# Performance work log

Measured on AMD Instinct MI355X. Metric: run time of the kernel, lower is better.

Reference implementation:

```python
import jax, jax.numpy as jnp
import numpy as np

B, N, C, E = 8, 4096, 128, 131072  # batch, nodes, channels (in==out), edges


def _linear_params(key, fan_in, fan_out):
    kw, kb = jax.random.split(key)
    s = 1.0 / np.sqrt(fan_in).astype(np.float32)
    W = jax.random.uniform(kw, (fan_in, fan_out), jnp.float32, -s, s)
    b = jax.random.uniform(kb, (fan_out,), jnp.float32, -s, s)
    return W, b


def setup_inputs() -> dict:
    key = jax.random.key(0)
    ks = jax.random.split(key, 6)
    x = jax.random.normal(ks[0], (B, N, C), jnp.float32)
    edge_index = jax.random.randint(ks[1], (2, E), 0, N, jnp.int64)
    W0, b0 = _linear_params(ks[2], C, C)        # lin0: in -> out
    W1, b1 = _linear_params(ks[3], 2 * C, C)    # lin1: 2*out -> out
    W2, b2 = _linear_params(ks[4], C, C)        # lin2: out -> out
    Wo, bo = _linear_params(ks[5], C, C)        # output: out -> out
    return {"x": x, "edge_index": edge_index, "W0": W0, "b0": b0,
            "W1": W1, "b1": b1, "W2": W2, "b2": b2, "Wo": Wo, "bo": bo}


def reference(x, edge_index, W0, b0, W1, b1, W2, b2, Wo, bo):
    n = x.shape[1]
    # symmetric 0/1 adjacency (duplicate edges collapse via .set), zero diagonal
    adj = jnp.zeros((n, n), x.dtype)
    adj = adj.at[edge_index[0], edge_index[1]].set(1.0)
    adj = adj.at[edge_index[1], edge_index[0]].set(1.0)
    diag = jnp.arange(n)
    adj = adj.at[diag, diag].set(0.0)
    h = x @ W0 + b0                               # [B, N, C]
    agg = jnp.einsum('ij,bjd->bid', adj, h)       # neighbor aggregation
    cat = jnp.concatenate([x, agg], axis=-1)      # [B, N, 2C]
    out = (cat @ W1 + b1) @ W2 + b2
    out = jax.nn.gelu(out, approximate=False) @ Wo + bo  # torch exact GELU
    return x + out
```

## Files before the change

kernel.cpp:

```cpp
#include <hip/hip_runtime.h>
#include <hip/hip_bf16.h>
#include <math.h>

#define NN 4096
#define BB 8
#define CC 128
#define EE 131072
#define M_ROWS (BB*NN)
#define DEG_CAP 512

typedef __attribute__((ext_vector_type(8))) short short8;
typedef __attribute__((ext_vector_type(4))) float f32x4;

__device__ __forceinline__ float bf2f(unsigned int u){
    union { unsigned int i; float f; } v; v.i = u << 16; return v.f;
}
__device__ __forceinline__ unsigned short f2bf(float f){
    union { float f; unsigned int i; } v; v.f = f;
    unsigned int u = v.i;
    unsigned int r = u + 0x7FFFu + ((u >> 16) & 1u);
    return (unsigned short)(r >> 16);
}

__device__ __forceinline__ int swz(int r, int k2 ){
    return r * 256 + (k2 ^ ((r & 7) << 4));
}

__global__ __launch_bounds__(256) void k_init(uint4* __restrict__ bits4,
                                              const float* __restrict__ x,
                                              unsigned short* __restrict__ xb,
                                              const float* __restrict__ W0, const float* __restrict__ W1,
                                              const float* __restrict__ W2, const float* __restrict__ Wo,
                                              unsigned short* __restrict__ Wt1a, unsigned short* __restrict__ Wt1b,
                                              unsigned short* __restrict__ Wt2,  unsigned short* __restrict__ Wto,
                                              unsigned short* __restrict__ W0bf){
    int bid = blockIdx.x, t = threadIdx.x;
    if (bid < 512){
        bits4[bid * 256 + t] = (uint4){0u, 0u, 0u, 0u};
        return;
    }
    if (bid < 2560){
        size_t e = (size_t)(bid - 512) * 2048 + t * 8;
        float4 lo = *((const float4*)(x + e));
        float4 hi = *((const float4*)(x + e + 4));
        ushort4 w0, w1;
        w0.x = f2bf(lo.x); w0.y = f2bf(lo.y); w0.z = f2bf(lo.z); w0.w = f2bf(lo.w);
        w1.x = f2bf(hi.x); w1.y = f2bf(hi.y); w1.z = f2bf(hi.z); w1.w = f2bf(hi.w);
        *((ushort4*)(xb + e)) = w0;
        *((ushort4*)(xb + e + 4)) = w1;
        return;
    }
    int idx = (bid - 2560) * 256 + t;
    int s = idx >> 14;
    int e = idx & 16383;
    int n = e >> 7, k = e & 127;
    float v; unsigned short* dst;
    switch (s){
        case 0:  v = W1[k*128+n];        dst = Wt1a; break;
        case 1:  v = W1[(128+k)*128+n];  dst = Wt1b; break;
        case 2:  v = W2[k*128+n];        dst = Wt2;  break;
        case 3:  v = Wo[k*128+n];        dst = Wto;  break;
        default: v = W0[n*128+k];        dst = W0bf; break;
    }
    dst[n*128+k] = f2bf(v);
}

__device__ __forceinline__ void stage_w(const unsigned short* __restrict__ Wt,
                                        unsigned short* Ws, int t){
    #pragma unroll
    for (int it = 0; it < 8; ++it){
        int g = it * 2048 + t * 8;
        int r = g >> 7, k = g & 127;
        uint4 v = *((const uint4*)(Wt + r * 128 + k));
        *((uint4*)((char*)Ws + swz(r, k * 2))) = v;
    }
}
__device__ __forceinline__ void stage_a_bf16(const unsigned short* __restrict__ src, int blockRow,
                                             unsigned short* As, int t){
    #pragma unroll
    for (int it = 0; it < 4; ++it){
        int g = it * 2048 + t * 8;
        int r = g >> 7, k = g & 127;
        uint4 v = *((const uint4*)(src + (size_t)(blockRow + r) * 128 + k));
        *((uint4*)((char*)As + swz(r, k * 2))) = v;
    }
}
__device__ __forceinline__ void mfma_pass(const unsigned short* As, const unsigned short* Ws,
                                          int wr, int wc, int l15, int lh, f32x4 acc[2][4]){
    #pragma unroll
    for (int ks = 0; ks < 4; ++ks){
        const int kc = ks * 32 + lh * 8;
        short8 af[2], bfv[4];
        #pragma unroll
        for (int m = 0; m < 2; m++){
            int r = wr + m * 16 + l15;
            af[m] = *((const short8*)((const char*)As + swz(r, kc * 2)));
        }
        #pragma unroll
        for (int n = 0; n < 4; n++){
            int r = wc + n * 16 + l15;
            bfv[n] = *((const short8*)((const char*)Ws + swz(r, kc * 2)));
        }
        #pragma unroll
        for (int m = 0; m < 2; m++)
            #pragma unroll
            for (int n = 0; n < 4; n++)
                acc[m][n] = __builtin_amdgcn_mfma_f32_16x16x32_bf16(af[m], bfv[n], acc[m][n], 0, 0, 0);
    }
}

__global__ __launch_bounds__(256) void k_scatter(const int* __restrict__ ei,
                                                 unsigned int* __restrict__ bits,
                                                 const unsigned short* __restrict__ W0bf,
                                                 const unsigned short* __restrict__ Wt1b,
                                                 const float* __restrict__ b0,
                                                 const float* __restrict__ W1,
                                                 unsigned short* __restrict__ Wtu,
                                                 float* __restrict__ c1){
    const int bid = blockIdx.x, t = threadIdx.x;
    if (bid < 512){
        int e = bid * 256 + t;
        int u = ei[e], v = ei[EE + e];
        atomicOr(&bits[u * 128 + (v >> 5)], 1u << (v & 31));
        atomicOr(&bits[v * 128 + (u >> 5)], 1u << (u & 31));
        return;
    }
    __shared__ unsigned short As[128*128];
    __shared__ unsigned short Ws[128*128];
    stage_w(W0bf, As, t);
    stage_w(Wt1b, Ws, t);
    __syncthreads();
    const int lane = t & 63, w = t >> 6;
    const int wr = w * 32;
    const int l15 = lane & 15, lh = lane >> 4;
    f32x4 acc[2][8];
    #pragma unroll
    for (int m = 0; m < 2; m++) for (int n = 0; n < 8; n++) acc[m][n] = (f32x4)(0.0f);
    #pragma unroll
    for (int ks = 0; ks < 4; ++ks){
        const int kc = ks * 32 + lh * 8;
        short8 af[2], bfv[8];
        #pragma unroll
        for (int m = 0; m < 2; m++){
            int r = wr + m * 16 + l15;
            af[m] = *((const short8*)((const char*)As + swz(r, kc * 2)));
        }
        #pragma unroll
        for (int n = 0; n < 8; n++){
            int r = n * 16 + l15;
            bfv[n] = *((const short8*)((const char*)Ws + swz(r, kc * 2)));
        }
        #pragma unroll
        for (int m = 0; m < 2; m++)
            #pragma unroll
            for (int n = 0; n < 8; n++)
                acc[m][n] = __builtin_amdgcn_mfma_f32_16x16x32_bf16(af[m], bfv[n], acc[m][n], 0, 0, 0);
    }
    #pragma unroll
    for (int m = 0; m < 2; m++){
        #pragma unroll
        for (int rr = 0; rr < 4; rr++){
            int r = wr + m * 16 + lh * 4 + rr;
            #pragma unroll
            for (int n = 0; n < 8; n++){
                int c = n * 16 + l15;
                Wtu[c * 128 + r] = f2bf(acc[m][n][rr]);
            }
        }
    }
    if (t < 128){
        float s = 0.f;
        #pragma unroll 8
        for (int k = 0; k < 128; k++)
            s += b0[k] * W1[(size_t)(128 + k) * 128 + t];
        c1[t] = s;
    }
}

__global__ __launch_bounds__(128) void k_csr(const unsigned int* __restrict__ bits,
                                             unsigned short* __restrict__ cols, int* __restrict__ deg){
    __shared__ int sc[128];
    int i = blockIdx.x, t = threadIdx.x;
    unsigned int w = bits[i * 128 + t];
    if (t == (i >> 5)) w &= ~(1u << (i & 31));
    int c = __popc(w);
    sc[t] = c; __syncthreads();
    int val = c;
    for (int off = 1; off < 128; off <<= 1){
        int add = (t >= off) ? sc[t - off] : 0;
        __syncthreads();
        val += add; sc[t] = val;
        __syncthreads();
    }
    int total = sc[127];
    int pos = val - c;
    unsigned int ww = w;
    while (ww){
        int b = __ffs(ww) - 1;
        ww &= ww - 1;
        if (pos < DEG_CAP) cols[(size_t)i * DEG_CAP + pos] = (unsigned short)(t * 32 + b);
        pos++;
    }
    if (t == 0) deg[i] = total < DEG_CAP ? total : DEG_CAP;
}

__device__ __forceinline__ void acc8u(uint4 u, float* a){
    a[0] += bf2f(u.x & 0xFFFFu); a[1] += bf2f(u.x >> 16);
    a[2] += bf2f(u.y & 0xFFFFu); a[3] += bf2f(u.y >> 16);
    a[4] += bf2f(u.z & 0xFFFFu); a[5] += bf2f(u.z >> 16);
    a[6] += bf2f(u.w & 0xFFFFu); a[7] += bf2f(u.w >> 16);
}

__global__ __launch_bounds__(256) void k_agg(const unsigned short* __restrict__ h,
                                             const unsigned short* __restrict__ cols,
                                             const int* __restrict__ deg,
                                             unsigned short* __restrict__ agg){
    __shared__ unsigned short scol[4][DEG_CAP];
    const int t = threadIdx.x;
    const int w = t >> 6, lane = t & 63;
    const int sub = lane >> 4, li = lane & 15;
    const int b = blockIdx.x & 7;
    const int i = ((blockIdx.x >> 3) << 2) + w;
    const int d = deg[i];
    const unsigned short* cl = cols + (size_t)i * DEG_CAP;
    for (int q = lane; q < d; q += 64) scol[w][q] = cl[q];

    const unsigned short* hb = h + (size_t)b * (NN*128) + li * 8;
    float a[8];
    #pragma unroll
    for (int c = 0; c < 8; c++) a[c] = 0.f;

    int n = sub;
    for (; n + 4 < d; n += 8){
        int j0 = scol[w][n], j1 = scol[w][n+4];
        uint4 u0 = *((const uint4*)(hb + ((size_t)j0 << 7)));
        uint4 u1 = *((const uint4*)(hb + ((size_t)j1 << 7)));
        acc8u(u0, a); acc8u(u1, a);
    }
    if (n < d){
        uint4 u0 = *((const uint4*)(hb + ((size_t)scol[w][n] << 7)));
        acc8u(u0, a);
    }
    #pragma unroll
    for (int c = 0; c < 8; c++){
        a[c] += __shfl_xor(a[c], 16);
        a[c] += __shfl_xor(a[c], 32);
    }
    if (sub == 0){
        uint4 o;
        o.x = (unsigned)f2bf(a[0]) | ((unsigned)f2bf(a[1]) << 16);
        o.y = (unsigned)f2bf(a[2]) | ((unsigned)f2bf(a[3]) << 16);
        o.z = (unsigned)f2bf(a[4]) | ((unsigned)f2bf(a[5]) << 16);
        o.w = (unsigned)f2bf(a[6]) | ((unsigned)f2bf(a[7]) << 16);
        *((uint4*)(agg + (size_t)b * (NN*128) + ((size_t)i << 7) + li * 8)) = o;
    }
}

__global__ __launch_bounds__(256) void k_mlp(const unsigned short* __restrict__ xb,
                                             const unsigned short* __restrict__ u,
                                             const unsigned short* __restrict__ Wt1a,
                                             const unsigned short* __restrict__ Wtu,
                                             const unsigned short* __restrict__ Wt2,
                                             const unsigned short* __restrict__ Wto,
                                             const float* __restrict__ c1,
                                             const float* __restrict__ b1,
                                             const float* __restrict__ b2,
                                             const float* __restrict__ bo,
                                             const int* __restrict__ deg,
                                             float* __restrict__ out){
    __shared__ unsigned short As[64*128];
    __shared__ unsigned short Ws[128*128];
    const int t = threadIdx.x;
    const int blockRow = blockIdx.x * 64;
    const int lane = t & 63, w = t >> 6;
    const int wr = (w >> 1) * 32, wc = (w & 1) * 64;
    const int l15 = lane & 15, lh = lane >> 4;

    f32x4 acc[2][4];
    #pragma unroll
    for (int m = 0; m < 2; m++) for (int n = 0; n < 4; n++) acc[m][n] = (f32x4)(0.0f);

    stage_a_bf16(xb, blockRow, As, t);
    stage_w(Wt1a, Ws, t);
    __syncthreads();
    mfma_pass(As, Ws, wr, wc, l15, lh, acc);

    f32x4 acc3[2][4];
    #pragma unroll
    for (int m = 0; m < 2; m++){
        #pragma unroll
        for (int rr = 0; rr < 4; rr++){
            int rl = wr + m * 16 + lh * 4 + rr;
            #pragma unroll
            for (int n = 0; n < 4; n++){
                int col = wc + n * 16 + l15;
                unsigned int us = *((const unsigned short*)((const char*)As + swz(rl, col * 2)));
                acc3[m][n][rr] = bf2f(us) + bo[col];
            }
        }
    }
    __syncthreads();

    stage_a_bf16(u, blockRow, As, t);
    stage_w(Wtu, Ws, t);
    __syncthreads();
    mfma_pass(As, Ws, wr, wc, l15, lh, acc);
    __syncthreads();

    #pragma unroll
    for (int m = 0; m < 2; m++){
        #pragma unroll
        for (int rr = 0; rr < 4; rr++){
            int rl = wr + m * 16 + lh * 4 + rr;
            int node = (blockRow + rl) & (NN - 1);
            float degf = (float)deg[node];
            #pragma unroll
            for (int n = 0; n < 4; n++){
                int col = wc + n * 16 + l15;
                float v = acc[m][n][rr] + b1[col] + degf * c1[col];
                *((unsigned short*)((char*)As + swz(rl, col * 2))) = f2bf(v);
            }
        }
    }
    stage_w(Wt2, Ws, t);
    __syncthreads();

    f32x4 acc2[2][4];
    #pragma unroll
    for (int m = 0; m < 2; m++) for (int n = 0; n < 4; n++) acc2[m][n] = (f32x4)(0.0f);
    mfma_pass(As, Ws, wr, wc, l15, lh, acc2);
    __syncthreads();

    #pragma unroll
    for (int m = 0; m < 2; m++){
        #pragma unroll
        for (int rr = 0; rr < 4; rr++){
            int rl = wr + m * 16 + lh * 4 + rr;
            #pragma unroll
            for (int n = 0; n < 4; n++){
                int col = wc + n * 16 + l15;
                float v = acc2[m][n][rr] + b2[col];
                v = 0.5f * v * (1.0f + erff(v * 0.70710678118f));
                *((unsigned short*)((char*)As + swz(rl, col * 2))) = f2bf(v);
            }
        }
    }
    stage_w(Wto, Ws, t);
    __syncthreads();

    mfma_pass(As, Ws, wr, wc, l15, lh, acc3);

    #pragma unroll
    for (int m = 0; m < 2; m++){
        #pragma unroll
        for (int rr = 0; rr < 4; rr++){
            int row = blockRow + wr + m * 16 + lh * 4 + rr;
            #pragma unroll
            for (int n = 0; n < 4; n++){
                int col = wc + n * 16 + l15;
                out[(size_t)row * 128 + col] = acc3[m][n][rr];
            }
        }
    }
}

extern "C" void kernel_launch(void* const* d_in, const int* in_sizes, int n_in,
                              void* d_out, int out_size, void* d_ws, size_t ws_size,
                              hipStream_t stream) {
    const float* x  = (const float*)d_in[0];
    const int*   ei = (const int*)d_in[1];
    const float* W0 = (const float*)d_in[2];
    const float* b0 = (const float*)d_in[3];
    const float* W1 = (const float*)d_in[4];
    const float* b1 = (const float*)d_in[5];
    const float* W2 = (const float*)d_in[6];
    const float* b2 = (const float*)d_in[7];
    const float* Wo = (const float*)d_in[8];
    const float* bo = (const float*)d_in[9];
    float* out = (float*)d_out;

    char* ws = (char*)d_ws;
    unsigned int* bits    = (unsigned int*)(ws + 0);
    unsigned short* cols  = (unsigned short*)(ws + 2097152);
    int*   deg            = (int*)(ws + 6291456);
    unsigned short* xb    = (unsigned short*)(ws + 6307840);
    unsigned short* ubuf  = (unsigned short*)(ws + 14696448);
    unsigned short* Wt1a  = (unsigned short*)(ws + 23085056);
    unsigned short* Wt1b  = (unsigned short*)(ws + 23085056 + 32768);
    unsigned short* Wt2   = (unsigned short*)(ws + 23085056 + 65536);
    unsigned short* Wto   = (unsigned short*)(ws + 23085056 + 98304);
    unsigned short* W0bf  = (unsigned short*)(ws + 23085056 + 131072);
    unsigned short* Wtu   = (unsigned short*)(ws + 23085056 + 163840);
    float* c1             = (float*)(ws + 23085056 + 196608);

    k_init<<<2880, 256, 0, stream>>>((uint4*)bits, x, xb, W0, W1, W2, Wo,
                                     Wt1a, Wt1b, Wt2, Wto, W0bf);
    k_scatter<<<513, 256, 0, stream>>>(ei, bits, W0bf, Wt1b, b0, W1, Wtu, c1);
    k_csr<<<NN, 128, 0, stream>>>(bits, cols, deg);
    k_agg<<<BB * (NN / 4), 256, 0, stream>>>(xb, cols, deg, ubuf);
    k_mlp<<<M_ROWS / 64, 256, 0, stream>>>(xb, ubuf, Wt1a, Wtu, Wt2, Wto,
                                           c1, b1, b2, bo, deg, out);
}
```

Baseline: 77.10 us.

## Fuse neighbor aggregation gather into the MLP kernel, dropping agg buffer

Removes the separate k_agg kernel and performs the sparse neighbor gather-sum directly inside k_mlp, writing aggregated rows into shared memory instead of a global intermediate buffer. Blocks are remapped to batch-interleaved order so that neighbouring blocks share node chunks. This saves a kernel launch and a global write and re-read of the aggregate. The trade-off is that the gather now runs inside the heavy MLP kernel with less parallelism per node (each wave handles 16 rows serially), which may expose latency and reduce occupancy.

```diff
diff --git a/kernel.cpp b/kernel.cpp
--- a/kernel.cpp
+++ b/kernel.cpp
@@ -75,13 +75,13 @@
         *((uint4*)((char*)Ws + swz(r, k * 2))) = v;
     }
 }
-__device__ __forceinline__ void stage_a_bf16(const unsigned short* __restrict__ src, int blockRow,
+__device__ __forceinline__ void stage_a_bf16(const unsigned short* __restrict__ src, size_t blockRow,
                                              unsigned short* As, int t){
     #pragma unroll
     for (int it = 0; it < 4; ++it){
         int g = it * 2048 + t * 8;
         int r = g >> 7, k = g & 127;
-        uint4 v = *((const uint4*)(src + (size_t)(blockRow + r) * 128 + k));
+        uint4 v = *((const uint4*)(src + (blockRow + r) * 128 + k));
         *((uint4*)((char*)As + swz(r, k * 2))) = v;
     }
 }
@@ -211,53 +211,9 @@
     a[6] += bf2f(u.w & 0xFFFFu); a[7] += bf2f(u.w >> 16);
 }
 
-__global__ __launch_bounds__(256) void k_agg(const unsigned short* __restrict__ h,
+__global__ __launch_bounds__(256) void k_mlp(const unsigned short* __restrict__ xb,
                                              const unsigned short* __restrict__ cols,
                                              const int* __restrict__ deg,
-                                             unsigned short* __restrict__ agg){
-    __shared__ unsigned short scol[4][DEG_CAP];
-    const int t = threadIdx.x;
-    const int w = t >> 6, lane = t & 63;
-    const int sub = lane >> 4, li = lane & 15;
-    const int b = blockIdx.x & 7;
-    const int i = ((blockIdx.x >> 3) << 2) + w;
-    const int d = deg[i];
-    const unsigned short* cl = cols + (size_t)i * DEG_CAP;
-    for (int q = lane; q < d; q += 64) scol[w][q] = cl[q];
-
-    const unsigned short* hb = h + (size_t)b * (NN*128) + li * 8;
-    float a[8];
-    #pragma unroll
-    for (int c = 0; c < 8; c++) a[c] = 0.f;
-
-    int n = sub;
-    for (; n + 4 < d; n += 8){
-        int j0 = scol[w][n], j1 = scol[w][n+4];
-        uint4 u0 = *((const uint4*)(hb + ((size_t)j0 << 7)));
-        uint4 u1 = *((const uint4*)(hb + ((size_t)j1 << 7)));
-        acc8u(u0, a); acc8u(u1, a);
-    }
-    if (n < d){
-        uint4 u0 = *((const uint4*)(hb + ((size_t)scol[w][n] << 7)));
-        acc8u(u0, a);
-    }
-    #pragma unroll
-    for (int c = 0; c < 8; c++){
-        a[c] += __shfl_xor(a[c], 16);
-        a[c] += __shfl_xor(a[c], 32);
-    }
-    if (sub == 0){
-        uint4 o;
-        o.x = (unsigned)f2bf(a[0]) | ((unsigned)f2bf(a[1]) << 16);
-        o.y = (unsigned)f2bf(a[2]) | ((unsigned)f2bf(a[3]) << 16);
-        o.z = (unsigned)f2bf(a[4]) | ((unsigned)f2bf(a[5]) << 16);
-        o.w = (unsigned)f2bf(a[6]) | ((unsigned)f2bf(a[7]) << 16);
-        *((uint4*)(agg + (size_t)b * (NN*128) + ((size_t)i << 7) + li * 8)) = o;
-    }
-}
-
-__global__ __launch_bounds__(256) void k_mlp(const unsigned short* __restrict__ xb,
-                                             const unsigned short* __restrict__ u,
                                              const unsigned short* __restrict__ Wt1a,
                                              const unsigned short* __restrict__ Wtu,
                                              const unsigned short* __restrict__ Wt2,
@@ -266,12 +222,13 @@
                                              const float* __restrict__ b1,
                                              const float* __restrict__ b2,
                                              const float* __restrict__ bo,
-                                             const int* __restrict__ deg,
                                              float* __restrict__ out){
     __shared__ unsigned short As[64*128];
     __shared__ unsigned short Ws[128*128];
     const int t = threadIdx.x;
-    const int blockRow = blockIdx.x * 64;
+    const int batch = blockIdx.x & 7;
+    const int chunk = blockIdx.x >> 3;
+    const size_t blockRow = (size_t)batch * NN + chunk * 64;
     const int lane = t & 63, w = t >> 6;
     const int wr = (w >> 1) * 32, wc = (w & 1) * 64;
     const int l15 = lane & 15, lh = lane >> 4;
@@ -301,9 +258,47 @@
     }
     __syncthreads();
 
-    stage_a_bf16(u, blockRow, As, t);
+    {
+        const int sub = lane >> 4, li = lane & 15;
+        const unsigned short* hb = xb + (size_t)batch * (NN*128) + li * 8;
+        const int row0 = w * 16;
+        for (int q = 0; q < 16; ++q){
+            int rl = row0 + q;
+            int node = chunk * 64 + rl;
+            int d = deg[node];
+            const unsigned short* cl = cols + (size_t)node * DEG_CAP;
+            float a[8];
+            #pragma unroll
+            for (int c = 0; c < 8; c++) a[c] = 0.f;
+            int n = sub;
+            for (; n + 4 < d; n += 8){
+                int j0 = cl[n], j1 = cl[n+4];
+                uint4 u0 = *((const uint4*)(hb + ((size_t)j0 << 7)));
+                uint4 u1 = *((const uint4*)(hb + ((size_t)j1 << 7)));
+                acc8u(u0, a); acc8u(u1, a);
+            }
+            if (n < d){
+                uint4 u0 = *((const uint4*)(hb + ((size_t)cl[n] << 7)));
+                acc8u(u0, a);
+            }
+            #pragma unroll
+            for (int c = 0; c < 8; c++){
+                a[c] += __shfl_xor(a[c], 16);
+                a[c] += __shfl_xor(a[c], 32);
+            }
+            if (sub == 0){
+                uint4 o;
+                o.x = (unsigned)f2bf(a[0]) | ((unsigned)f2bf(a[1]) << 16);
+                o.y = (unsigned)f2bf(a[2]) | ((unsigned)f2bf(a[3]) << 16);
+                o.z = (unsigned)f2bf(a[4]) | ((unsigned)f2bf(a[5]) << 16);
+                o.w = (unsigned)f2bf(a[6]) | ((unsigned)f2bf(a[7]) << 16);
+                *((uint4*)((char*)As + swz(rl, li * 16))) = o;
+            }
+        }
+    }
     stage_w(Wtu, Ws, t);
     __syncthreads();
+
     mfma_pass(As, Ws, wr, wc, l15, lh, acc);
     __syncthreads();
 
@@ -312,7 +307,7 @@
         #pragma unroll
         for (int rr = 0; rr < 4; rr++){
             int rl = wr + m * 16 + lh * 4 + rr;
-            int node = (blockRow + rl) & (NN - 1);
+            int node = chunk * 64 + rl;
             float degf = (float)deg[node];
             #pragma unroll
             for (int n = 0; n < 4; n++){
@@ -354,11 +349,11 @@
     for (int m = 0; m < 2; m++){
         #pragma unroll
         for (int rr = 0; rr < 4; rr++){
-            int row = blockRow + wr + m * 16 + lh * 4 + rr;
+            size_t row = blockRow + wr + m * 16 + lh * 4 + rr;
             #pragma unroll
             for (int n = 0; n < 4; n++){
                 int col = wc + n * 16 + l15;
-                out[(size_t)row * 128 + col] = acc3[m][n][rr];
+                out[row * 128 + col] = acc3[m][n][rr];
             }
         }
     }
@@ -384,20 +379,18 @@
     unsigned short* cols  = (unsigned short*)(ws + 2097152);
     int*   deg            = (int*)(ws + 6291456);
     unsigned short* xb    = (unsigned short*)(ws + 6307840);
-    unsigned short* ubuf  = (unsigned short*)(ws + 14696448);
-    unsigned short* Wt1a  = (unsigned short*)(ws + 23085056);
-    unsigned short* Wt1b  = (unsigned short*)(ws + 23085056 + 32768);
-    unsigned short* Wt2   = (unsigned short*)(ws + 23085056 + 65536);
-    unsigned short* Wto   = (unsigned short*)(ws + 23085056 + 98304);
-    unsigned short* W0bf  = (unsigned short*)(ws + 23085056 + 131072);
-    unsigned short* Wtu   = (unsigned short*)(ws + 23085056 + 163840);
-    float* c1             = (float*)(ws + 23085056 + 196608);
+    unsigned short* Wt1a  = (unsigned short*)(ws + 14696448);
+    unsigned short* Wt1b  = (unsigned short*)(ws + 14696448 + 32768);
+    unsigned short* Wt2   = (unsigned short*)(ws + 14696448 + 65536);
+    unsigned short* Wto   = (unsigned short*)(ws + 14696448 + 98304);
+    unsigned short* W0bf  = (unsigned short*)(ws + 14696448 + 131072);
+    unsigned short* Wtu   = (unsigned short*)(ws + 14696448 + 163840);
+    float* c1             = (float*)(ws + 14696448 + 196608);
 
     k_init<<<2880, 256, 0, stream>>>((uint4*)bits, x, xb, W0, W1, W2, Wo,
                                      Wt1a, Wt1b, Wt2, Wto, W0bf);
     k_scatter<<<513, 256, 0, stream>>>(ei, bits, W0bf, Wt1b, b0, W1, Wtu, c1);
     k_csr<<<NN, 128, 0, stream>>>(bits, cols, deg);
-    k_agg<<<BB * (NN / 4), 256, 0, stream>>>(xb, cols, deg, ubuf);
-    k_mlp<<<M_ROWS / 64, 256, 0, stream>>>(xb, ubuf, Wt1a, Wtu, Wt2, Wto,
-                                           c1, b1, b2, bo, deg, out);
-}
+    k_mlp<<<M_ROWS / 64, 256, 0, stream>>>(xb, cols, deg, Wt1a, Wtu, Wt2, Wto,
+                                           c1, b1, b2, bo, out);
+}
```

After: 109.3 us. 41.8% more time.

## Fuse CSR construction into aggregation kernel using wave-level bitmask scan

Applied to the files above, without the earlier changes.

Drops the separate k_csr launch and its global cols buffer. Each wavefront of k_agg now reads its node's adjacency bitmask row, builds the neighbour list in shared memory with a shuffle-based prefix scan, and writes deg once (only from batch 0). Every batch repeats the row expansion, which adds redundant ALU work. The gather loop is also unrolled from 2 to 4 loads in flight to raise memory-level parallelism. This removes one launch and a global write and read round trip. The risk is that deg is written by k_agg and read later by k_mlp, which relies on launch order.

```diff
diff --git a/kernel.cpp b/kernel.cpp
--- a/kernel.cpp
+++ b/kernel.cpp
@@ -75,13 +75,13 @@
         *((uint4*)((char*)Ws + swz(r, k * 2))) = v;
     }
 }
-__device__ __forceinline__ void stage_a_bf16(const unsigned short* __restrict__ src, int blockRow,
+__device__ __forceinline__ void stage_a_bf16(const unsigned short* __restrict__ src, size_t blockRow,
                                              unsigned short* As, int t){
     #pragma unroll
     for (int it = 0; it < 4; ++it){
         int g = it * 2048 + t * 8;
         int r = g >> 7, k = g & 127;
-        uint4 v = *((const uint4*)(src + (size_t)(blockRow + r) * 128 + k));
+        uint4 v = *((const uint4*)(src + (blockRow + r) * 128 + k));
         *((uint4*)((char*)As + swz(r, k * 2))) = v;
     }
 }
@@ -177,33 +177,6 @@
     }
 }
 
-__global__ __launch_bounds__(128) void k_csr(const unsigned int* __restrict__ bits,
-                                             unsigned short* __restrict__ cols, int* __restrict__ deg){
-    __shared__ int sc[128];
-    int i = blockIdx.x, t = threadIdx.x;
-    unsigned int w = bits[i * 128 + t];
-    if (t == (i >> 5)) w &= ~(1u << (i & 31));
-    int c = __popc(w);
-    sc[t] = c; __syncthreads();
-    int val = c;
-    for (int off = 1; off < 128; off <<= 1){
-        int add = (t >= off) ? sc[t - off] : 0;
-        __syncthreads();
-        val += add; sc[t] = val;
-        __syncthreads();
-    }
-    int total = sc[127];
-    int pos = val - c;
-    unsigned int ww = w;
-    while (ww){
-        int b = __ffs(ww) - 1;
-        ww &= ww - 1;
-        if (pos < DEG_CAP) cols[(size_t)i * DEG_CAP + pos] = (unsigned short)(t * 32 + b);
-        pos++;
-    }
-    if (t == 0) deg[i] = total < DEG_CAP ? total : DEG_CAP;
-}
-
 __device__ __forceinline__ void acc8u(uint4 u, float* a){
     a[0] += bf2f(u.x & 0xFFFFu); a[1] += bf2f(u.x >> 16);
     a[2] += bf2f(u.y & 0xFFFFu); a[3] += bf2f(u.y >> 16);
@@ -212,39 +185,68 @@
 }
 
 __global__ __launch_bounds__(256) void k_agg(const unsigned short* __restrict__ h,
-                                             const unsigned short* __restrict__ cols,
-                                             const int* __restrict__ deg,
+                                             const unsigned int* __restrict__ bits,
+                                             int* __restrict__ deg,
                                              unsigned short* __restrict__ agg){
     __shared__ unsigned short scol[4][DEG_CAP];
     const int t = threadIdx.x;
     const int w = t >> 6, lane = t & 63;
-    const int sub = lane >> 4, li = lane & 15;
     const int b = blockIdx.x & 7;
     const int i = ((blockIdx.x >> 3) << 2) + w;
-    const int d = deg[i];
-    const unsigned short* cl = cols + (size_t)i * DEG_CAP;
-    for (int q = lane; q < d; q += 64) scol[w][q] = cl[q];
-
+
+    uint2 wv = *((const uint2*)(bits + i * 128 + lane * 2));
+    unsigned int w0 = wv.x, w1 = wv.y;
+    int dw = i >> 5;
+    if (dw == lane * 2)          w0 &= ~(1u << (i & 31));
+    else if (dw == lane * 2 + 1) w1 &= ~(1u << (i & 31));
+    int c = __popc(w0) + __popc(w1);
+    int incl = c;
+    #pragma unroll
+    for (int off = 1; off < 64; off <<= 1){
+        int nb = __shfl_up(incl, off);
+        if (lane >= off) incl += nb;
+    }
+    int total = __shfl(incl, 63);
+    int pos = incl - c;
+    int base = lane * 64;
+    unsigned int ww = w0;
+    while (ww){
+        int bit = __ffs(ww) - 1; ww &= ww - 1;
+        if (pos < DEG_CAP) scol[w][pos] = (unsigned short)(base + bit);
+        pos++;
+    }
+    ww = w1; base += 32;
+    while (ww){
+        int bit = __ffs(ww) - 1; ww &= ww - 1;
+        if (pos < DEG_CAP) scol[w][pos] = (unsigned short)(base + bit);
+        pos++;
+    }
+    const int d = total < DEG_CAP ? total : DEG_CAP;
+    if (b == 0 && lane == 0) deg[i] = d;
+
+    const int sub = lane >> 4, li = lane & 15;
     const unsigned short* hb = h + (size_t)b * (NN*128) + li * 8;
     float a[8];
     #pragma unroll
-    for (int c = 0; c < 8; c++) a[c] = 0.f;
+    for (int q = 0; q < 8; q++) a[q] = 0.f;
 
     int n = sub;
-    for (; n + 4 < d; n += 8){
-        int j0 = scol[w][n], j1 = scol[w][n+4];
+    for (; n + 12 < d; n += 16){
+        int j0 = scol[w][n], j1 = scol[w][n+4], j2 = scol[w][n+8], j3 = scol[w][n+12];
         uint4 u0 = *((const uint4*)(hb + ((size_t)j0 << 7)));
         uint4 u1 = *((const uint4*)(hb + ((size_t)j1 << 7)));
-        acc8u(u0, a); acc8u(u1, a);
-    }
-    if (n < d){
+        uint4 u2 = *((const uint4*)(hb + ((size_t)j2 << 7)));
+        uint4 u3 = *((const uint4*)(hb + ((size_t)j3 << 7)));
+        acc8u(u0, a); acc8u(u1, a); acc8u(u2, a); acc8u(u3, a);
+    }
+    for (; n < d; n += 4){
         uint4 u0 = *((const uint4*)(hb + ((size_t)scol[w][n] << 7)));
         acc8u(u0, a);
     }
     #pragma unroll
-    for (int c = 0; c < 8; c++){
-        a[c] += __shfl_xor(a[c], 16);
-        a[c] += __shfl_xor(a[c], 32);
+    for (int q = 0; q < 8; q++){
+        a[q] += __shfl_xor(a[q], 16);
+        a[q] += __shfl_xor(a[q], 32);
     }
     if (sub == 0){
         uint4 o;
@@ -271,7 +273,7 @@
     __shared__ unsigned short As[64*128];
     __shared__ unsigned short Ws[128*128];
     const int t = threadIdx.x;
-    const int blockRow = blockIdx.x * 64;
+    const size_t blockRow = (size_t)blockIdx.x * 64;
     const int lane = t & 63, w = t >> 6;
     const int wr = (w >> 1) * 32, wc = (w & 1) * 64;
     const int l15 = lane & 15, lh = lane >> 4;
@@ -312,7 +314,7 @@
         #pragma unroll
         for (int rr = 0; rr < 4; rr++){
             int rl = wr + m * 16 + lh * 4 + rr;
-            int node = (blockRow + rl) & (NN - 1);
+            int node = (int)((blockRow + rl) & (NN - 1));
             float degf = (float)deg[node];
             #pragma unroll
             for (int n = 0; n < 4; n++){
@@ -354,11 +356,11 @@
     for (int m = 0; m < 2; m++){
         #pragma unroll
         for (int rr = 0; rr < 4; rr++){
-            int row = blockRow + wr + m * 16 + lh * 4 + rr;
+            size_t row = blockRow + wr + m * 16 + lh * 4 + rr;
             #pragma unroll
             for (int n = 0; n < 4; n++){
                 int col = wc + n * 16 + l15;
-                out[(size_t)row * 128 + col] = acc3[m][n][rr];
+                out[row * 128 + col] = acc3[m][n][rr];
             }
         }
     }
@@ -381,23 +383,21 @@
 
     char* ws = (char*)d_ws;
     unsigned int* bits    = (unsigned int*)(ws + 0);
-    unsigned short* cols  = (unsigned short*)(ws + 2097152);
-    int*   deg            = (int*)(ws + 6291456);
-    unsigned short* xb    = (unsigned short*)(ws + 6307840);
-    unsigned short* ubuf  = (unsigned short*)(ws + 14696448);
-    unsigned short* Wt1a  = (unsigned short*)(ws + 23085056);
-    unsigned short* Wt1b  = (unsigned short*)(ws + 23085056 + 32768);
-    unsigned short* Wt2   = (unsigned short*)(ws + 23085056 + 65536);
-    unsigned short* Wto   = (unsigned short*)(ws + 23085056 + 98304);
-    unsigned short* W0bf  = (unsigned short*)(ws + 23085056 + 131072);
-    unsigned short* Wtu   = (unsigned short*)(ws + 23085056 + 163840);
-    float* c1             = (float*)(ws + 23085056 + 196608);
+    int*   deg            = (int*)(ws + 2097152);
+    unsigned short* xb    = (unsigned short*)(ws + 2113536);
+    unsigned short* ubuf  = (unsigned short*)(ws + 10502144);
+    unsigned short* Wt1a  = (unsigned short*)(ws + 18890752);
+    unsigned short* Wt1b  = (unsigned short*)(ws + 18890752 + 32768);
+    unsigned short* Wt2   = (unsigned short*)(ws + 18890752 + 65536);
+    unsigned short* Wto   = (unsigned short*)(ws + 18890752 + 98304);
+    unsigned short* W0bf  = (unsigned short*)(ws + 18890752 + 131072);
+    unsigned short* Wtu   = (unsigned short*)(ws + 18890752 + 163840);
+    float* c1             = (float*)(ws + 18890752 + 196608);
 
     k_init<<<2880, 256, 0, stream>>>((uint4*)bits, x, xb, W0, W1, W2, Wo,
                                      Wt1a, Wt1b, Wt2, Wto, W0bf);
     k_scatter<<<513, 256, 0, stream>>>(ei, bits, W0bf, Wt1b, b0, W1, Wtu, c1);
-    k_csr<<<NN, 128, 0, stream>>>(bits, cols, deg);
-    k_agg<<<BB * (NN / 4), 256, 0, stream>>>(xb, cols, deg, ubuf);
+    k_agg<<<BB * (NN / 4), 256, 0, stream>>>(xb, bits, deg, ubuf);
     k_mlp<<<M_ROWS / 64, 256, 0, stream>>>(xb, ubuf, Wt1a, Wtu, Wt2, Wto,
                                            c1, b1, b2, bo, deg, out);
 }
```

Measured after the change: 75.28 us, median of 3. 1.02x faster.
